# Kernel optimization log

Measured on AMD Instinct MI355X. Metric: run time of the kernel, lower is better.

The kernel has to match this reference:

```python
import jax, jax.numpy as jnp
import numpy as np

B, L, H, I = 2, 256, 768, 1536


def setup_inputs() -> dict:
    key = jax.random.key(0)
    ks = jax.random.split(key, 10)
    s = 0.02
    return {
        "hidden_state": jax.random.normal(ks[0], (B, L, H), dtype=jnp.float32),
        "start_w": jax.random.normal(ks[1], (H,), dtype=jnp.float32) * s,
        "start_b": jnp.zeros((), dtype=jnp.float32),
        "end_w": jax.random.normal(ks[2], (H,), dtype=jnp.float32) * s,
        "end_b": jnp.zeros((), dtype=jnp.float32),
        "w1": jax.random.normal(ks[3], (2 * H, I), dtype=jnp.float32) * s,
        "b1": jnp.zeros((I,), dtype=jnp.float32),
        "w2": jax.random.normal(ks[4], (I,), dtype=jnp.float32) * s,
        "b2": jnp.zeros((), dtype=jnp.float32),
    }


def reference(hidden_state, start_w, start_b, end_w, end_b, w1, b1, w2, b2):
    # start/end token logits: (B, L)
    start_logits = jnp.einsum("blh,h->bl", hidden_state, start_w) + start_b
    end_logits = jnp.einsum("blh,h->bl", hidden_state, end_w) + end_b

    # Linear(concat(start_extend, end_extend)) == start @ w1[:H] + end @ w1[H:]
    # (algebraically identical; avoids materializing the (B,L,L,2H) concat)
    w1_start, w1_end = w1[:H], w1[H:]
    a = jnp.einsum("bsh,hi->bsi", hidden_state, w1_start)  # (B, L, I)
    c = jnp.einsum("bth,hi->bti", hidden_state, w1_end)    # (B, L, I)
    inter = jax.nn.gelu(a[:, :, None, :] + c[:, None, :, :] + b1,
                        approximate=False)                 # (B, L, L, I)
    span_logits = jnp.einsum("bsti,i->bst", inter, w2) + b2  # (B, L, L)

    return start_logits, end_logits, span_logits
```

## Files before the change

kernel.cpp:

```cpp
#include <hip/hip_runtime.h>
#include <math.h>

#define NB 2
#define NL 256
#define NH 768
#define NI 1536
#define NM (NB * NL)

typedef __attribute__((ext_vector_type(8))) short bf16x8;
typedef __attribute__((ext_vector_type(4))) float f32x4;
typedef __attribute__((ext_vector_type(4))) unsigned int u32x4;

#if __has_builtin(__builtin_amdgcn_exp2f)
#define FAST_EXP2(x) __builtin_amdgcn_exp2f(x)
#else
#define FAST_EXP2(x) exp2f(x)
#endif
#if __has_builtin(__builtin_amdgcn_rcpf)
#define FAST_RCP(x) __builtin_amdgcn_rcpf(x)
#else
#define FAST_RCP(x) (1.0f / (x))
#endif

#define KQ (-2.4554669f)

__device__ __forceinline__ unsigned short f2bf(float f) {
  unsigned int u = __builtin_bit_cast(unsigned int, f);
  u += 0x7FFFu + ((u >> 16) & 1u);
  return (unsigned short)(u >> 16);
}
__device__ __forceinline__ unsigned int pack2(float lo, float hi) {
  return (unsigned int)f2bf(lo) | ((unsigned int)f2bf(hi) << 16);
}
__device__ __forceinline__ float bits2f(unsigned int u) {
  return __builtin_bit_cast(float, u);
}

__global__ __launch_bounds__(512) void gemm_mfma(
    const float* __restrict__ hs, const float* __restrict__ w1,
    const float* __restrict__ b1, const float* __restrict__ w2,
    const float* __restrict__ sw, const float* __restrict__ sb,
    const float* __restrict__ ew, const float* __restrict__ eb,
    float* __restrict__ aOut, unsigned int* __restrict__ cE,
    float* __restrict__ out) {
  constexpr int BM = 64, BN = 96, BK = 32;
  __shared__ short A_lds[BM * BK];
  __shared__ short B_lds[BN * BK];
  __shared__ float ls_s[4][2], ls_e[4][2];

  const int tid = threadIdx.x;

  if (blockIdx.z == 2) {
    const int gid = blockIdx.x * 16 + blockIdx.y;
    const int g = tid >> 7;
    const int l = tid & 127;
    const int m = gid * 4 + g;
    const float* row = hs + (size_t)m * NH;
    float accs = 0.f, acce = 0.f;
    for (int h = l; h < NH; h += 128) {
      float v = row[h];
      accs = fmaf(v, sw[h], accs);
      acce = fmaf(v, ew[h], acce);
    }
    for (int off = 32; off > 0; off >>= 1) {
      accs += __shfl_down(accs, off, 64);
      acce += __shfl_down(acce, off, 64);
    }
    if ((tid & 63) == 0) {
      ls_s[g][(tid >> 6) & 1] = accs;
      ls_e[g][(tid >> 6) & 1] = acce;
    }
    __syncthreads();
    if (l == 0) {
      out[m]      = ls_s[g][0] + ls_s[g][1] + sb[0];
      out[NM + m] = ls_e[g][0] + ls_e[g][1] + eb[0];
    }
    return;
  }

  const int mode = blockIdx.z;
  const float* __restrict__ W = w1 + (size_t)mode * NH * NI;
  const int m0 = blockIdx.x * BM;
  const int n0 = blockIdx.y * BN;
  const int lane = tid & 63;
  const int wid = tid >> 6;
  const int wr = wid >> 1;
  const int wc = wid & 1;

  const int ar  = tid >> 3;
  const int ac  = (tid & 7) * 4;
  const int bkq = (tid >> 5) * 2;
  const int bnl = tid & 31;

  f32x4 acc[3] = {};

  float4 av = *reinterpret_cast<const float4*>(hs + (size_t)(m0 + ar) * NH + ac);
  float bv[2][3];
#pragma unroll
  for (int j = 0; j < 2; ++j) {
    const float* pb = W + (size_t)(bkq + j) * NI + n0 + bnl;
#pragma unroll
    for (int nn = 0; nn < 3; ++nn) bv[j][nn] = pb[nn * 32];
  }

  for (int k0 = 0; k0 < NH; k0 += BK) {
    __syncthreads();
    {
      uint2 v;
      v.x = pack2(av.x, av.y);
      v.y = pack2(av.z, av.w);
      const int off = ar * 64 + ((((ac >> 3) & 3) ^ (ar & 3)) << 4) + ((ac & 4) << 1);
      *reinterpret_cast<uint2*>(reinterpret_cast<char*>(A_lds) + off) = v;
    }
#pragma unroll
    for (int nn = 0; nn < 3; ++nn) {
      const int n = bnl + nn * 32;
      unsigned int v = pack2(bv[0][nn], bv[1][nn]);
      const int off = n * 64 + (((bkq >> 3) ^ (n & 3)) << 4) + ((bkq * 2) & 12);
      *reinterpret_cast<unsigned int*>(reinterpret_cast<char*>(B_lds) + off) = v;
    }
    __syncthreads();
    const int kn = k0 + BK;
    if (kn < NH) {
      av = *reinterpret_cast<const float4*>(hs + (size_t)(m0 + ar) * NH + kn + ac);
#pragma unroll
      for (int j = 0; j < 2; ++j) {
        const float* pb = W + (size_t)(kn + bkq + j) * NI + n0 + bnl;
#pragma unroll
        for (int nn = 0; nn < 3; ++nn) bv[j][nn] = pb[nn * 32];
      }
    }
    const int lr = lane & 15, ls = lane >> 4;
    bf16x8 af, bf[3];
    {
      const int row = wr * 16 + lr;
      const int off = row * 64 + ((ls ^ (row & 3)) << 4);
      af = *reinterpret_cast<const bf16x8*>(reinterpret_cast<const char*>(A_lds) + off);
    }
#pragma unroll
    for (int nt = 0; nt < 3; ++nt) {
      const int nrow = wc * 48 + nt * 16 + lr;
      const int off = nrow * 64 + ((ls ^ (nrow & 3)) << 4);
      bf[nt] = *reinterpret_cast<const bf16x8*>(reinterpret_cast<const char*>(B_lds) + off);
    }
#pragma unroll
    for (int nt = 0; nt < 3; ++nt)
      acc[nt] = __builtin_amdgcn_mfma_f32_16x16x32_bf16(af, bf[nt], acc[nt], 0, 0, 0);
  }

  const int lr = lane & 15, lq = lane >> 4;
  if (mode == 0) {
    const int mb = m0 + wr * 16 + lq * 4;
#pragma unroll
    for (int nt = 0; nt < 3; ++nt) {
      const int n = n0 + wc * 48 + nt * 16 + lr;
      const float bias = b1[n];
#pragma unroll
      for (int r = 0; r < 4; ++r)
        aOut[(size_t)(mb + r) * NI + n] = acc[nt][r] + bias;
    }
  } else {
    const int b = m0 >> 8;
    const int tb = (m0 & (NL - 1)) + wr * 16 + lq * 4;
#pragma unroll
    for (int nt = 0; nt < 3; ++nt) {
      const int i = n0 + wc * 48 + nt * 16 + lr;
      const float wv = w2[i];
      unsigned int* dst = cE + ((size_t)b * NI + i) * NL + tb;
      f32x4 v = acc[nt];
      u32x4 pk;
      pk.x = pack2(v[0] * wv, FAST_EXP2(KQ * v[0]));
      pk.y = pack2(v[1] * wv, FAST_EXP2(KQ * v[1]));
      pk.z = pack2(v[2] * wv, FAST_EXP2(KQ * v[2]));
      pk.w = pack2(v[3] * wv, FAST_EXP2(KQ * v[3]));
      *reinterpret_cast<u32x4*>(dst) = pk;
    }
  }
}

__global__ __launch_bounds__(256, 2) void span_kernel(
    const float* __restrict__ aRow,
    const unsigned int* __restrict__ cE,
    const float* __restrict__ w2,
    const float* __restrict__ b2,
    float* __restrict__ out) {
  const int blk = blockIdx.x;
  const int sg  = blk >> 3;
  const int te  = blk & 7;
  const int s0  = sg * 2;
  const int b   = s0 >> 8;
  const int tbase = te * 32;
  const int tid = threadIdx.x;
  const int t8  = tid & 7;
  const int q   = tid >> 3;
  const int lane = tid & 63;
  const int w    = tid >> 6;

  __shared__ float4 aw4[NI + 32];
  __shared__ float4 red[4][2][8];

  const float* a0p = aRow + (size_t)s0 * NI;
  const float* a1p = a0p + NI;
  for (int i = tid; i < NI; i += 256) {
    float a0 = a0p[i], a1 = a1p[i], wv = w2[i];
    aw4[i + i / 48] = make_float4(a0 * wv, a1 * wv,
                                  FAST_EXP2(KQ * a0), FAST_EXP2(KQ * a1));
  }
  __syncthreads();

  const unsigned int* cb = cE + ((size_t)b * NI + q * 48) * NL + tbase + t8 * 4;
  const float4* awq = aw4 + q * 49;

  f32x4 acc0 = {0.f, 0.f, 0.f, 0.f};
  f32x4 acc1 = {0.f, 0.f, 0.f, 0.f};

#pragma unroll 4
  for (int ii = 0; ii < 48; ++ii) {
    u32x4 cv = *reinterpret_cast<const u32x4*>(cb);
    float4 A = awq[ii];
    float cw0 = bits2f(cv.x << 16), E0 = bits2f(cv.x & 0xFFFF0000u);
    float cw1 = bits2f(cv.y << 16), E1 = bits2f(cv.y & 0xFFFF0000u);
    float cw2 = bits2f(cv.z << 16), E2 = bits2f(cv.z & 0xFFFF0000u);
    float cw3 = bits2f(cv.w << 16), E3 = bits2f(cv.w & 0xFFFF0000u);
    {
      float n0 = A.x + cw0, n1 = A.x + cw1;
      float n2 = A.x + cw2, n3 = A.x + cw3;
      float d0 = fmaf(A.z, E0, 1.f), d1 = fmaf(A.z, E1, 1.f);
      float d2 = fmaf(A.z, E2, 1.f), d3 = fmaf(A.z, E3, 1.f);
      float mA = d0 * d1, mB = d2 * d3;
      float r = FAST_RCP(mA * mB);
      float rA = r * mB, rB = r * mA;
      acc0[0] = fmaf(n0, rA * d1, acc0[0]);
      acc0[1] = fmaf(n1, rA * d0, acc0[1]);
      acc0[2] = fmaf(n2, rB * d3, acc0[2]);
      acc0[3] = fmaf(n3, rB * d2, acc0[3]);
    }
    {
      float n0 = A.y + cw0, n1 = A.y + cw1;
      float n2 = A.y + cw2, n3 = A.y + cw3;
      float d0 = fmaf(A.w, E0, 1.f), d1 = fmaf(A.w, E1, 1.f);
      float d2 = fmaf(A.w, E2, 1.f), d3 = fmaf(A.w, E3, 1.f);
      float mA = d0 * d1, mB = d2 * d3;
      float r = FAST_RCP(mA * mB);
      float rA = r * mB, rB = r * mA;
      acc1[0] = fmaf(n0, rA * d1, acc1[0]);
      acc1[1] = fmaf(n1, rA * d0, acc1[1]);
      acc1[2] = fmaf(n2, rB * d3, acc1[2]);
      acc1[3] = fmaf(n3, rB * d2, acc1[3]);
    }
    cb += NL;
  }

#pragma unroll
  for (int k = 0; k < 4; ++k) {
    acc0[k] += __shfl_xor(acc0[k], 8, 64);
    acc0[k] += __shfl_xor(acc0[k], 16, 64);
    acc0[k] += __shfl_xor(acc0[k], 32, 64);
    acc1[k] += __shfl_xor(acc1[k], 8, 64);
    acc1[k] += __shfl_xor(acc1[k], 16, 64);
    acc1[k] += __shfl_xor(acc1[k], 32, 64);
  }
  if (lane < 8) {
    red[w][0][lane] = make_float4(acc0[0], acc0[1], acc0[2], acc0[3]);
    red[w][1][lane] = make_float4(acc1[0], acc1[1], acc1[2], acc1[3]);
  }
  __syncthreads();
  if (tid < 16) {
    const int s = tid >> 3;
    const int tt = tid & 7;
    float4 v0 = red[0][s][tt];
    float4 v1 = red[1][s][tt];
    float4 v2 = red[2][s][tt];
    float4 v3 = red[3][s][tt];
    const float bb = b2[0];
    float4 o;
    o.x = (v0.x + v1.x) + (v2.x + v3.x) + bb;
    o.y = (v0.y + v1.y) + (v2.y + v3.y) + bb;
    o.z = (v0.z + v1.z) + (v2.z + v3.z) + bb;
    o.w = (v0.w + v1.w) + (v2.w + v3.w) + bb;
    *reinterpret_cast<float4*>(out + 2 * NM + (size_t)(s0 + s) * NL + tbase + tt * 4) = o;
  }
}

extern "C" void kernel_launch(void* const* d_in, const int* in_sizes, int n_in,
                              void* d_out, int out_size, void* d_ws, size_t ws_size,
                              hipStream_t stream) {
  const float* hs = (const float*)d_in[0];
  const float* sw = (const float*)d_in[1];
  const float* sb = (const float*)d_in[2];
  const float* ew = (const float*)d_in[3];
  const float* eb = (const float*)d_in[4];
  const float* w1 = (const float*)d_in[5];
  const float* b1 = (const float*)d_in[6];
  const float* w2 = (const float*)d_in[7];
  const float* b2 = (const float*)d_in[8];
  float* out = (float*)d_out;

  float* a = (float*)d_ws;
  unsigned int* cE = (unsigned int*)((float*)d_ws + (size_t)NM * NI);

  dim3 ggrid(NM / 64, NI / 96, 3);
  gemm_mfma<<<ggrid, 512, 0, stream>>>(hs, w1, b1, w2, sw, sb, ew, eb, a, cE, out);

  span_kernel<<<2048, 256, 0, stream>>>(a, cE, w2, b2, out);
}
```

Baseline: 62.05 us.

## Process four s-rows per span block with bf16-packed shared A operands

Each span_kernel block now handles four s rows instead of two, halving the grid and reusing every loaded cE vector across four rows. This cuts global/L2 traffic for cE per output. To keep the shared-memory footprint the same, the per-row a*w2 and exp terms are stored packed as bf16 pairs rather than fp32. The trade-offs are lower precision on the A-side operands, more registers per thread (which may reduce occupancy) and fewer blocks (1024) to spread across the GPU.

```diff
diff --git a/kernel.cpp b/kernel.cpp
--- a/kernel.cpp
+++ b/kernel.cpp
@@ -187,7 +187,7 @@
   const int blk = blockIdx.x;
   const int sg  = blk >> 3;
   const int te  = blk & 7;
-  const int s0  = sg * 2;
+  const int s0  = sg * 4;
   const int b   = s0 >> 8;
   const int tbase = te * 32;
   const int tid = threadIdx.x;
@@ -196,60 +196,62 @@
   const int lane = tid & 63;
   const int w    = tid >> 6;
 
-  __shared__ float4 aw4[NI + 32];
-  __shared__ float4 red[4][2][8];
+  __shared__ u32x4 aw4[NI + 32];
+  __shared__ float4 red[4][4][8];
 
   const float* a0p = aRow + (size_t)s0 * NI;
-  const float* a1p = a0p + NI;
   for (int i = tid; i < NI; i += 256) {
-    float a0 = a0p[i], a1 = a1p[i], wv = w2[i];
-    aw4[i + i / 48] = make_float4(a0 * wv, a1 * wv,
-                                  FAST_EXP2(KQ * a0), FAST_EXP2(KQ * a1));
+    float a0 = a0p[i], a1 = a0p[NI + i], a2 = a0p[2 * NI + i], a3 = a0p[3 * NI + i];
+    float wv = w2[i];
+    u32x4 pk;
+    pk.x = pack2(a0 * wv, a1 * wv);
+    pk.y = pack2(a2 * wv, a3 * wv);
+    pk.z = pack2(FAST_EXP2(KQ * a0), FAST_EXP2(KQ * a1));
+    pk.w = pack2(FAST_EXP2(KQ * a2), FAST_EXP2(KQ * a3));
+    aw4[i + i / 48] = pk;
   }
   __syncthreads();
 
   const unsigned int* cb = cE + ((size_t)b * NI + q * 48) * NL + tbase + t8 * 4;
-  const float4* awq = aw4 + q * 49;
+  const u32x4* awq = aw4 + q * 49;
 
   f32x4 acc0 = {0.f, 0.f, 0.f, 0.f};
   f32x4 acc1 = {0.f, 0.f, 0.f, 0.f};
+  f32x4 acc2 = {0.f, 0.f, 0.f, 0.f};
+  f32x4 acc3 = {0.f, 0.f, 0.f, 0.f};
+
+#define SBLK(ACC, AWU, EAU, HALF)                                   \
+  {                                                                 \
+    float aw_ = bits2f(HALF ? ((AWU) & 0xFFFF0000u) : ((AWU) << 16)); \
+    float Ea_ = bits2f(HALF ? ((EAU) & 0xFFFF0000u) : ((EAU) << 16)); \
+    float n0 = aw_ + cw0, n1 = aw_ + cw1;                           \
+    float n2 = aw_ + cw2, n3 = aw_ + cw3;                           \
+    float d0 = fmaf(Ea_, E0, 1.f), d1 = fmaf(Ea_, E1, 1.f);         \
+    float d2 = fmaf(Ea_, E2, 1.f), d3 = fmaf(Ea_, E3, 1.f);         \
+    float mA = d0 * d1, mB = d2 * d3;                               \
+    float r = FAST_RCP(mA * mB);                                    \
+    float rA = r * mB, rB = r * mA;                                 \
+    ACC[0] = fmaf(n0, rA * d1, ACC[0]);                             \
+    ACC[1] = fmaf(n1, rA * d0, ACC[1]);                             \
+    ACC[2] = fmaf(n2, rB * d3, ACC[2]);                             \
+    ACC[3] = fmaf(n3, rB * d2, ACC[3]);                             \
+  }
 
 #pragma unroll 4
   for (int ii = 0; ii < 48; ++ii) {
     u32x4 cv = *reinterpret_cast<const u32x4*>(cb);
-    float4 A = awq[ii];
+    u32x4 A = awq[ii];
     float cw0 = bits2f(cv.x << 16), E0 = bits2f(cv.x & 0xFFFF0000u);
     float cw1 = bits2f(cv.y << 16), E1 = bits2f(cv.y & 0xFFFF0000u);
     float cw2 = bits2f(cv.z << 16), E2 = bits2f(cv.z & 0xFFFF0000u);
     float cw3 = bits2f(cv.w << 16), E3 = bits2f(cv.w & 0xFFFF0000u);
-    {
-      float n0 = A.x + cw0, n1 = A.x + cw1;
-      float n2 = A.x + cw2, n3 = A.x + cw3;
-      float d0 = fmaf(A.z, E0, 1.f), d1 = fmaf(A.z, E1, 1.f);
-      float d2 = fmaf(A.z, E2, 1.f), d3 = fmaf(A.z, E3, 1.f);
-      float mA = d0 * d1, mB = d2 * d3;
-      float r = FAST_RCP(mA * mB);
-      float rA = r * mB, rB = r * mA;
-      acc0[0] = fmaf(n0, rA * d1, acc0[0]);
-      acc0[1] = fmaf(n1, rA * d0, acc0[1]);
-      acc0[2] = fmaf(n2, rB * d3, acc0[2]);
-      acc0[3] = fmaf(n3, rB * d2, acc0[3]);
-    }
-    {
-      float n0 = A.y + cw0, n1 = A.y + cw1;
-      float n2 = A.y + cw2, n3 = A.y + cw3;
-      float d0 = fmaf(A.w, E0, 1.f), d1 = fmaf(A.w, E1, 1.f);
-      float d2 = fmaf(A.w, E2, 1.f), d3 = fmaf(A.w, E3, 1.f);
-      float mA = d0 * d1, mB = d2 * d3;
-      float r = FAST_RCP(mA * mB);
-      float rA = r * mB, rB = r * mA;
-      acc1[0] = fmaf(n0, rA * d1, acc1[0]);
-      acc1[1] = fmaf(n1, rA * d0, acc1[1]);
-      acc1[2] = fmaf(n2, rB * d3, acc1[2]);
-      acc1[3] = fmaf(n3, rB * d2, acc1[3]);
-    }
+    SBLK(acc0, A.x, A.z, 0)
+    SBLK(acc1, A.x, A.z, 1)
+    SBLK(acc2, A.y, A.w, 0)
+    SBLK(acc3, A.y, A.w, 1)
     cb += NL;
   }
+#undef SBLK
 
 #pragma unroll
   for (int k = 0; k < 4; ++k) {
@@ -259,13 +261,21 @@
     acc1[k] += __shfl_xor(acc1[k], 8, 64);
     acc1[k] += __shfl_xor(acc1[k], 16, 64);
     acc1[k] += __shfl_xor(acc1[k], 32, 64);
+    acc2[k] += __shfl_xor(acc2[k], 8, 64);
+    acc2[k] += __shfl_xor(acc2[k], 16, 64);
+    acc2[k] += __shfl_xor(acc2[k], 32, 64);
+    acc3[k] += __shfl_xor(acc3[k], 8, 64);
+    acc3[k] += __shfl_xor(acc3[k], 16, 64);
+    acc3[k] += __shfl_xor(acc3[k], 32, 64);
   }
   if (lane < 8) {
     red[w][0][lane] = make_float4(acc0[0], acc0[1], acc0[2], acc0[3]);
     red[w][1][lane] = make_float4(acc1[0], acc1[1], acc1[2], acc1[3]);
+    red[w][2][lane] = make_float4(acc2[0], acc2[1], acc2[2], acc2[3]);
+    red[w][3][lane] = make_float4(acc3[0], acc3[1], acc3[2], acc3[3]);
   }
   __syncthreads();
-  if (tid < 16) {
+  if (tid < 32) {
     const int s = tid >> 3;
     const int tt = tid & 7;
     float4 v0 = red[0][s][tt];
@@ -302,5 +312,5 @@
   dim3 ggrid(NM / 64, NI / 96, 3);
   gemm_mfma<<<ggrid, 512, 0, stream>>>(hs, w1, b1, w2, sw, sb, ew, eb, a, cE, out);
 
-  span_kernel<<<2048, 256, 0, stream>>>(a, cE, w2, b2, out);
-}
+  span_kernel<<<1024, 256, 0, stream>>>(a, cE, w2, b2, out);
+}
```

After: 63.24 us. Within noise of the previous version (+1.9%).
